# Optimization experiments

Measured on AMD Instinct MI355X. Metric: run time of the kernel, lower is better.

The kernel has to match this reference:

```python
import jax, jax.numpy as jnp
import numpy as np

N = 100_000   # nodes
E = 1_600_000 # edges
C = 64        # in = hidden = out channels
H = 8         # heads
D = C // H    # head_dim = 8
R = 4         # relations
L = 2         # layers


def setup_inputs() -> dict:
    key = jax.random.key(0)
    ks = jax.random.split(key, 10)
    sc = 1.0 / np.sqrt(C)  # xavier-ish scale
    return {
        "x": jax.random.normal(ks[0], (N, C), jnp.float32),
        "edge_index": jax.random.randint(ks[1], (2, E), 0, N),
        "edge_type": jax.random.randint(ks[2], (E,), 0, R),
        "W_Q": jax.random.normal(ks[3], (L, R, H, C, D), jnp.float32) * sc,
        "W_K": jax.random.normal(ks[4], (L, R, H, C, D), jnp.float32) * sc,
        "W_V": jax.random.normal(ks[5], (L, R, H, C, D), jnp.float32) * sc,
        "W_concat": jax.random.normal(ks[6], (L, R, H * D, C), jnp.float32) * sc,
        "sem_w": jax.random.normal(ks[7], (L, C), jnp.float32) * sc,
        "sem_b": jnp.zeros((L,), jnp.float32),
        "W_self": jax.random.normal(ks[8], (L, C, C), jnp.float32) * sc,
        "ln_g": jnp.ones((L, C), jnp.float32),
        "ln_b": jnp.zeros((L, C), jnp.float32),
    }


def _layer(x, src, dst, edge_type, WQ, WK, WV, Wcat, sw, sb, Ws, g, b):
    inv_sqrt_d = 1.0 / np.sqrt(D)
    rel_msgs = []
    for r in range(R):  # small fixed relation loop
        mask = (edge_type == r).astype(x.dtype)             # (E,)
        Q = jnp.einsum('nc,hcd->nhd', x, WQ[r])             # (N,H,D)
        K = jnp.einsum('nc,hcd->nhd', x, WK[r])
        V = jnp.einsum('nc,hcd->nhd', x, WV[r])
        # edge-wise QK energy, leaky_relu(0.01), scatter-add into dst node
        energy = jnp.einsum('ehd,ehd->eh', Q[dst], K[src]) * inv_sqrt_d
        energy = jax.nn.leaky_relu(energy)                  # (E,H)
        alpha_n = jax.ops.segment_sum(energy * mask[:, None], dst,
                                      num_segments=N)       # (N,H)
        alpha = jax.nn.softmax(alpha_n, axis=0)             # softmax over nodes
        w = alpha[dst] * mask[:, None]                      # (E,H)
        m = jax.ops.segment_sum(w[:, :, None] * V[src], dst,
                                num_segments=N)             # (N,H,D)
        rel_msgs.append(m.reshape(N, H * D) @ Wcat[r])      # (N,C)
    stacked = jnp.stack(rel_msgs)                           # (R,N,C)
    beta = jax.nn.softmax(stacked @ sw + sb, axis=0)        # (R,N) semantic attn
    agg = jnp.einsum('rn,rnc->nc', beta, stacked)           # (N,C)
    y = x + jax.nn.gelu(x @ Ws + agg, approximate=False)
    mu = y.mean(-1, keepdims=True)
    var = y.var(-1, keepdims=True)
    return (y - mu) / jnp.sqrt(var + 1e-5) * g + b


def reference(x, edge_index, edge_type, W_Q, W_K, W_V, W_concat,
              sem_w, sem_b, W_self, ln_g, ln_b):
    src, dst = edge_index[0], edge_index[1]  # PyG source_to_target: j=row0, i=row1
    for l in range(L):
        x = _layer(x, src, dst, edge_type, W_Q[l], W_K[l], W_V[l], W_concat[l],
                   sem_w[l], sem_b[l], W_self[l], ln_g[l], ln_b[l])
        # inter-layer dropout omitted (inference / eval mode)
    return x
```

## Files before the change

### kernel.cpp

```cpp
#include <hip/hip_runtime.h>
#include <hip/hip_bf16.h>

#define NN 100000
#define EE 1600000
#define RRR 4
#define HHH 8
#define NT 400000
#define GG 782
#define SHIFT 9
#define NBLK 512
#define CHUNK 3125
#define BMAX 2560

typedef unsigned int u32;
typedef unsigned short u16;
typedef __attribute__((ext_vector_type(8))) short bf16x8;
typedef __attribute__((ext_vector_type(4))) float f32x4;

static constexpr size_t OFF_KV   = 0;
static constexpr size_t OFF_Q    = 25600000;
static constexpr size_t OFF_S    = 76800000;
static constexpr size_t OFF_AL   = 128000000;
static constexpr size_t OFF_PW   = 140800000;
static constexpr size_t OFF_PART = 141100000;
static constexpr size_t OFF_FIN  = 141110000;
static constexpr size_t OFF_CW   = 141120000;
static constexpr size_t OFF_ROWP = 141365504;
static constexpr size_t OFF_EDG  = 142965512;
static constexpr size_t OFF_LG   = 149400000;
static constexpr size_t OFF_BSTORE = OFF_S;
static constexpr size_t OFF_HIST   = OFF_S + 8000000;
static constexpr size_t OFF_OFFA   = OFF_S + 16000000;
static constexpr size_t OFF_BASE   = OFF_S + 24000000;

__device__ inline u16 f2bf(float f){
  union { __hip_bfloat16 h; u16 u; } cv; cv.h = __float2bfloat16(f); return cv.u;
}
__device__ inline float bf2f(u16 u){ return __uint_as_float(((u32)u) << 16); }

__global__ __launch_bounds__(256) void k_histA(const int* __restrict__ dst, const int* __restrict__ typ,
                                               u32* __restrict__ Hist){
  __shared__ u32 h[GG];
  int b = blockIdx.x, t = threadIdx.x;
  for (int g = t; g < GG; g += 256) h[g] = 0u;
  __syncthreads();
  int e0 = b * CHUNK;
  for (int e = e0 + t; e < e0 + CHUNK; e += 256){
    int seg = typ[e] * NN + dst[e];
    atomicAdd(&h[seg >> SHIFT], 1u);
  }
  __syncthreads();
  for (int g = t; g < GG; g += 256) Hist[(size_t)b * GG + g] = h[g];
}

__global__ __launch_bounds__(1024) void k_base(const u32* __restrict__ Hist, u32* __restrict__ Base,
                                               u32* __restrict__ rowp){
  __shared__ u32 tot[GG];
  int t = threadIdx.x;
  if (t < GG){
    u32 s = 0;
    for (int b = 0; b < NBLK; b++) s += Hist[(size_t)b * GG + t];
    tot[t] = s;
  }
  __syncthreads();
  if (t == 0){
    u32 acc = 0;
    for (int g = 0; g < GG; g++){ u32 c = tot[g]; Base[g] = acc; acc += c; }
    Base[GG] = acc;
    rowp[NT] = EE;
  }
}

__global__ __launch_bounds__(512) void k_off(const u32* __restrict__ Hist, const u32* __restrict__ Base,
                                             u32* __restrict__ Off){
  __shared__ u32 v[NBLK];
  int g = blockIdx.x, t = threadIdx.x;
  v[t] = Hist[(size_t)t * GG + g];
  __syncthreads();
  if (t == 0){
    u32 acc = Base[g];
    for (int b = 0; b < NBLK; b++){ u32 c = v[b]; v[b] = acc; acc += c; }
  }
  __syncthreads();
  Off[(size_t)g * NBLK + t] = v[t];
}

__global__ __launch_bounds__(256) void k_fill(const int* __restrict__ src, const int* __restrict__ dst,
                                              const int* __restrict__ typ, const u32* __restrict__ Off,
                                              u32* __restrict__ bstore){
  __shared__ u32 cur[GG];
  int b = blockIdx.x, t = threadIdx.x;
  for (int g = t; g < GG; g += 256) cur[g] = Off[(size_t)g * NBLK + b];
  __syncthreads();
  int e0 = b * CHUNK;
  for (int e = e0 + t; e < e0 + CHUNK; e += 256){
    int seg = typ[e] * NN + dst[e];
    u32 pos = atomicAdd(&cur[seg >> SHIFT], 1u);
    bstore[pos] = ((u32)(seg & 511) << 17) | (u32)src[e];
  }
}

__global__ __launch_bounds__(256) void k_sortD(const u32* __restrict__ bstore, const u32* __restrict__ Base,
                                               u32* __restrict__ rowp, u32* __restrict__ edges){
  __shared__ u32 ent[BMAX];
  __shared__ u32 binc[512], bexc[512];
  int g = blockIdx.x, t = threadIdx.x;
  u32 base = Base[g];
  u32 cnt = Base[g + 1] - base;
  if (cnt > (u32)BMAX) cnt = (u32)BMAX;
  for (int i = t; i < 512; i += 256) binc[i] = 0u;
  __syncthreads();
  for (u32 i = t; i < cnt; i += 256){
    u32 v = bstore[base + i];
    ent[i] = v;
    atomicAdd(&binc[v >> 17], 1u);
  }
  __syncthreads();
  if (t == 0){
    u32 acc = 0;
    #pragma unroll 8
    for (int s = 0; s < 512; s++){ u32 c = binc[s]; bexc[s] = acc; binc[s] = acc; acc += c; }
  }
  __syncthreads();
  for (int s = t; s < 512; s += 256){
    int seg = g * 512 + s;
    if (seg < NT) rowp[seg] = base + bexc[s];
  }
  __syncthreads();
  for (u32 i = t; i < cnt; i += 256){
    u32 v = ent[i];
    u32 p = atomicAdd(&binc[v >> 17], 1u);
    edges[base + p] = v & 0x1FFFFu;
  }
}

__global__ __launch_bounds__(256) void k_repackbf(const float* __restrict__ WQ, const float* __restrict__ WK,
                                                  const float* __restrict__ WV, const float* __restrict__ Wcat,
                                                  const float* __restrict__ Wself, u16* __restrict__ pwB){
  int t = blockIdx.x * 256 + threadIdx.x;
  if (t >= 2 * 17 * 4096) return;
  int l = t / (17 * 4096), rem = t % (17 * 4096);
  int mat = rem >> 12, idx = rem & 4095;
  int out = idx >> 6, c = idx & 63;
  float v;
  if (mat < 12){
    int kind = mat >> 2, r = mat & 3;
    int h = out >> 3, d = out & 7;
    const float* Wsrc = (kind == 0) ? WQ : (kind == 1) ? WK : WV;
    v = Wsrc[((((l * RRR + r) * HHH + h) * 64) + c) * 8 + d];
  } else if (mat == 12){
    v = Wself[(l * 64 + c) * 64 + out];
  } else {
    int r = mat - 13;
    v = Wcat[(((l * RRR + r) * 64) + c) * 64 + out];
  }
  pwB[t] = f2bf(v);
}

__global__ __launch_bounds__(512) void k_cw(const float* __restrict__ Wcat, const float* __restrict__ semw,
                                            float* __restrict__ cw){
  int t = threadIdx.x;
  int l = t >> 8, r = (t >> 6) & 3, k = t & 63;
  const float* wp = Wcat + (((size_t)(l * RRR + r) * 64) + k) * 64;
  const float* sp = semw + l * 64;
  float s = 0.f;
  #pragma unroll 8
  for (int c = 0; c < 64; c++) s += wp[c] * sp[c];
  cw[t] = s;
}


__global__ __launch_bounds__(256) void k_qkv(const float* __restrict__ x,
                                             const u16* __restrict__ pwQ, const u16* __restrict__ pwK,
                                             const u16* __restrict__ pwV,
                                             u16* __restrict__ Qr, u32* __restrict__ kvp){
  __shared__ u16 xa[64][72];
  __shared__ u16 wt[3][64][72];
  int t = threadIdx.x;
  int n0 = blockIdx.x * 64;
  {
    int row = t >> 2, c0 = (t & 3) * 16;
    int n = n0 + row;
    float4 v0 = {}, v1 = {}, v2 = {}, v3 = {};
    if (n < NN){
      const float4* xp = (const float4*)(x + (size_t)n * 64 + c0);
      v0 = xp[0]; v1 = xp[1]; v2 = xp[2]; v3 = xp[3];
    }
    ushort4* dp = (ushort4*)&xa[row][c0];
    dp[0] = make_ushort4(f2bf(v0.x), f2bf(v0.y), f2bf(v0.z), f2bf(v0.w));
    dp[1] = make_ushort4(f2bf(v1.x), f2bf(v1.y), f2bf(v1.z), f2bf(v1.w));
    dp[2] = make_ushort4(f2bf(v2.x), f2bf(v2.y), f2bf(v2.z), f2bf(v2.w));
    dp[3] = make_ushort4(f2bf(v3.x), f2bf(v3.y), f2bf(v3.z), f2bf(v3.w));
  }
  {
    const u32* p0 = (const u32*)pwQ;
    const u32* p1 = (const u32*)pwK;
    const u32* p2 = (const u32*)pwV;
    for (int idx = t; idx < 3 * 2048; idx += 256){
      int m = idx >> 11, rem = idx & 2047;
      int out = rem >> 5, cc = rem & 31;
      u32 w = (m == 0) ? p0[rem] : (m == 1) ? p1[rem] : p2[rem];
      *(u32*)&wt[m][out][cc * 2] = w;
    }
  }
  __syncthreads();
  int w = t >> 6, lane = t & 63;
  int ra = w * 16 + (lane & 15);
  int kg = (lane >> 4) * 8;
  int cb = lane & 15;
  int rb = (lane >> 4) * 4;
  bf16x8 a0 = *(const bf16x8*)&xa[ra][kg];
  bf16x8 a1 = *(const bf16x8*)&xa[ra][32 + kg];
  f32x4 z = {0.f, 0.f, 0.f, 0.f};
  {
    f32x4 acc[4] = {z, z, z, z};
    #pragma unroll
    for (int t4 = 0; t4 < 4; t4++){
      bf16x8 b0 = *(const bf16x8*)&wt[0][t4 * 16 + cb][kg];
      bf16x8 b1 = *(const bf16x8*)&wt[0][t4 * 16 + cb][32 + kg];
      acc[t4] = __builtin_amdgcn_mfma_f32_16x16x32_bf16(a0, b0, acc[t4], 0, 0, 0);
      acc[t4] = __builtin_amdgcn_mfma_f32_16x16x32_bf16(a1, b1, acc[t4], 0, 0, 0);
    }
    #pragma unroll
    for (int t4 = 0; t4 < 4; t4++){
      #pragma unroll
      for (int i = 0; i < 4; i++){
        int n = n0 + w * 16 + rb + i;
        if (n < NN) Qr[(size_t)n * 64 + t4 * 16 + cb] = f2bf(acc[t4][i]);
      }
    }
  }
  {
    f32x4 ak[4] = {z, z, z, z};
    f32x4 av[4] = {z, z, z, z};
    #pragma unroll
    for (int t4 = 0; t4 < 4; t4++){
      bf16x8 bk0 = *(const bf16x8*)&wt[1][t4 * 16 + cb][kg];
      bf16x8 bk1 = *(const bf16x8*)&wt[1][t4 * 16 + cb][32 + kg];
      bf16x8 bv0 = *(const bf16x8*)&wt[2][t4 * 16 + cb][kg];
      bf16x8 bv1 = *(const bf16x8*)&wt[2][t4 * 16 + cb][32 + kg];
      ak[t4] = __builtin_amdgcn_mfma_f32_16x16x32_bf16(a0, bk0, ak[t4], 0, 0, 0);
      ak[t4] = __builtin_amdgcn_mfma_f32_16x16x32_bf16(a1, bk1, ak[t4], 0, 0, 0);
      av[t4] = __builtin_amdgcn_mfma_f32_16x16x32_bf16(a0, bv0, av[t4], 0, 0, 0);
      av[t4] = __builtin_amdgcn_mfma_f32_16x16x32_bf16(a1, bv1, av[t4], 0, 0, 0);
    }
    #pragma unroll
    for (int t4 = 0; t4 < 4; t4++){
      #pragma unroll
      for (int i = 0; i < 4; i++){
        int n = n0 + w * 16 + rb + i;
        if (n < NN) kvp[(size_t)n * 64 + t4 * 16 + cb] = (u32)f2bf(ak[t4][i]) | ((u32)f2bf(av[t4][i]) << 16);
      }
    }
  }
}

__global__ __launch_bounds__(256) void k_self(const float* __restrict__ x, const u16* __restrict__ pwS,
                                              u16* __restrict__ outb){
  __shared__ u16 xa[64][72];
  __shared__ u16 wt[64][72];
  int t = threadIdx.x;
  int n0 = blockIdx.x * 64;
  {
    int row = t >> 2, c0 = (t & 3) * 16;
    int n = n0 + row;
    float4 v0 = {}, v1 = {}, v2 = {}, v3 = {};
    if (n < NN){
      const float4* xp = (const float4*)(x + (size_t)n * 64 + c0);
      v0 = xp[0]; v1 = xp[1]; v2 = xp[2]; v3 = xp[3];
    }
    ushort4* dp = (ushort4*)&xa[row][c0];
    dp[0] = make_ushort4(f2bf(v0.x), f2bf(v0.y), f2bf(v0.z), f2bf(v0.w));
    dp[1] = make_ushort4(f2bf(v1.x), f2bf(v1.y), f2bf(v1.z), f2bf(v1.w));
    dp[2] = make_ushort4(f2bf(v2.x), f2bf(v2.y), f2bf(v2.z), f2bf(v2.w));
    dp[3] = make_ushort4(f2bf(v3.x), f2bf(v3.y), f2bf(v3.z), f2bf(v3.w));
  }
  {
    const u32* p0 = (const u32*)pwS;
    for (int idx = t; idx < 2048; idx += 256){
      int out = idx >> 5, cc = idx & 31;
      *(u32*)&wt[out][cc * 2] = p0[idx];
    }
  }
  __syncthreads();
  int w = t >> 6, lane = t & 63;
  int ra = w * 16 + (lane & 15);
  int kg = (lane >> 4) * 8;
  int cb = lane & 15;
  int rb = (lane >> 4) * 4;
  bf16x8 a0 = *(const bf16x8*)&xa[ra][kg];
  bf16x8 a1 = *(const bf16x8*)&xa[ra][32 + kg];
  f32x4 z = {0.f, 0.f, 0.f, 0.f};
  f32x4 acc[4] = {z, z, z, z};
  #pragma unroll
  for (int t4 = 0; t4 < 4; t4++){
    bf16x8 b0 = *(const bf16x8*)&wt[t4 * 16 + cb][kg];
    bf16x8 b1 = *(const bf16x8*)&wt[t4 * 16 + cb][32 + kg];
    acc[t4] = __builtin_amdgcn_mfma_f32_16x16x32_bf16(a0, b0, acc[t4], 0, 0, 0);
    acc[t4] = __builtin_amdgcn_mfma_f32_16x16x32_bf16(a1, b1, acc[t4], 0, 0, 0);
  }
  #pragma unroll
  for (int t4 = 0; t4 < 4; t4++){
    #pragma unroll
    for (int i = 0; i < 4; i++){
      int n = n0 + w * 16 + rb + i;
      if (n < NN) outb[(size_t)n * 64 + t4 * 16 + cb] = f2bf(acc[t4][i]);
    }
  }
}

__global__ __launch_bounds__(256) void k_gather(const u32* __restrict__ edges, const u32* __restrict__ rowpR,
                                                const u32* __restrict__ kvp, const u16* __restrict__ Qr,
                                                u16* __restrict__ Sr, float* __restrict__ alphaR){
  int wid = threadIdx.x >> 6, lane = threadIdx.x & 63;
  int half = lane >> 5;
  int i = lane & 31;
  int n = blockIdx.x * 4 + wid;
  u32 qp = *(const u32*)&Qr[(size_t)n * 64 + 2 * i];
  float q0 = bf2f((u16)(qp & 0xFFFFu));
  float q1 = bf2f((u16)(qp >> 16));
  u32 beg = rowpR[n], end = rowpR[n + 1];
  float sa0 = 0.f, sa1 = 0.f, aa = 0.f;
  const float isd = 0.35355339059327373f;
  for (u32 base = beg; base < end; base += 64){
    u32 cnt = (end - base < 64u) ? (end - base) : 64u;
    u32 eidx = (base + (u32)lane < end) ? edges[base + lane] : 0u;
    u32 j = 0;
    for (; j + 8 <= cnt; j += 8){
      int s0 = __shfl((int)eidx, (int)(j + half));
      int s1 = __shfl((int)eidx, (int)(j + 2 + half));
      int s2 = __shfl((int)eidx, (int)(j + 4 + half));
      int s3 = __shfl((int)eidx, (int)(j + 6 + half));
      uint2 w0 = *(const uint2*)&kvp[(size_t)s0 * 64 + 2 * i];
      uint2 w1 = *(const uint2*)&kvp[(size_t)s1 * 64 + 2 * i];
      uint2 w2 = *(const uint2*)&kvp[(size_t)s2 * 64 + 2 * i];
      uint2 w3 = *(const uint2*)&kvp[(size_t)s3 * 64 + 2 * i];
      float p0 = q0 * bf2f((u16)(w0.x & 0xFFFFu)) + q1 * bf2f((u16)(w0.y & 0xFFFFu));
      float p1 = q0 * bf2f((u16)(w1.x & 0xFFFFu)) + q1 * bf2f((u16)(w1.y & 0xFFFFu));
      float p2 = q0 * bf2f((u16)(w2.x & 0xFFFFu)) + q1 * bf2f((u16)(w2.y & 0xFFFFu));
      float p3 = q0 * bf2f((u16)(w3.x & 0xFFFFu)) + q1 * bf2f((u16)(w3.y & 0xFFFFu));
      p0 += __shfl_xor(p0, 1); p1 += __shfl_xor(p1, 1); p2 += __shfl_xor(p2, 1); p3 += __shfl_xor(p3, 1);
      p0 += __shfl_xor(p0, 2); p1 += __shfl_xor(p1, 2); p2 += __shfl_xor(p2, 2); p3 += __shfl_xor(p3, 2);
      float e0 = p0 * isd; e0 = (e0 > 0.f) ? e0 : 0.01f * e0;
      float e1 = p1 * isd; e1 = (e1 > 0.f) ? e1 : 0.01f * e1;
      float e2 = p2 * isd; e2 = (e2 > 0.f) ? e2 : 0.01f * e2;
      float e3 = p3 * isd; e3 = (e3 > 0.f) ? e3 : 0.01f * e3;
      aa += (e0 + e1) + (e2 + e3);
      sa0 += (bf2f((u16)(w0.x >> 16)) + bf2f((u16)(w1.x >> 16))) +
             (bf2f((u16)(w2.x >> 16)) + bf2f((u16)(w3.x >> 16)));
      sa1 += (bf2f((u16)(w0.y >> 16)) + bf2f((u16)(w1.y >> 16))) +
             (bf2f((u16)(w2.y >> 16)) + bf2f((u16)(w3.y >> 16)));
    }
    for (; j < cnt; j += 2){
      u32 jj = j + (u32)half;
      float mk = (jj < cnt) ? 1.f : 0.f;
      u32 js = (jj < cnt) ? jj : (cnt - 1);
      int s = __shfl((int)eidx, (int)js);
      uint2 w = *(const uint2*)&kvp[(size_t)s * 64 + 2 * i];
      float p = q0 * bf2f((u16)(w.x & 0xFFFFu)) + q1 * bf2f((u16)(w.y & 0xFFFFu));
      p += __shfl_xor(p, 1);
      p += __shfl_xor(p, 2);
      float e = p * isd; e = (e > 0.f) ? e : 0.01f * e;
      aa += e * mk;
      sa0 += bf2f((u16)(w.x >> 16)) * mk;
      sa1 += bf2f((u16)(w.y >> 16)) * mk;
    }
  }
  sa0 += __shfl_xor(sa0, 32);
  sa1 += __shfl_xor(sa1, 32);
  aa  += __shfl_xor(aa, 32);
  if (half == 0){
    ushort2 o; o.x = f2bf(sa0); o.y = f2bf(sa1);
    *(ushort2*)&Sr[(size_t)n * 64 + 2 * i] = o;
    if ((i & 3) == 0) alphaR[(size_t)n * 8 + (i >> 2)] = aa;
  }
}

__global__ __launch_bounds__(256) void k_stats1(const float* __restrict__ alpha, float2* __restrict__ part){
  int r = blockIdx.y;
  int chunk = blockIdx.x;
  const int per = (NN + 31) / 32;
  int nbeg = chunk * per;
  int nend = nbeg + per; if (nend > NN) nend = NN;
  int t = threadIdx.x;
  int h = t & 7;
  int g = t >> 3;
  float m = -1e30f, s = 0.f;
  for (int n = nbeg + g; n < nend; n += 32){
    float a = alpha[((size_t)r * NN + n) * 8 + h];
    if (a > m){ s *= expf(m - a); m = a; }
    s += expf(a - m);
  }
  __shared__ float sm[256], ss[256];
  sm[t] = m; ss[t] = s; __syncthreads();
  for (int off = 128; off >= 8; off >>= 1){
    if (t < off){
      float m2 = sm[t + off], s2 = ss[t + off];
      float M = fmaxf(sm[t], m2);
      ss[t] = ss[t] * expf(sm[t] - M) + s2 * expf(m2 - M);
      sm[t] = M;
    }
    __syncthreads();
  }
  if (t < 8) part[(r * 8 + t) * 32 + chunk] = make_float2(sm[t], ss[t]);
}

__global__ void k_stats2(const float2* __restrict__ part, float2* __restrict__ fin){
  int col = threadIdx.x;
  if (col < 32){
    float M = -1e30f, S = 0.f;
    for (int i = 0; i < 32; i++){
      float2 p = part[col * 32 + i];
      float Mn = fmaxf(M, p.x);
      S = S * expf(M - Mn) + p.y * expf(p.x - Mn);
      M = Mn;
    }
    fin[col] = make_float2(M, 1.f / S);
  }
}

__global__ __launch_bounds__(256) void k_msg(const u16* __restrict__ S, const float* __restrict__ alpha,
                                             const float2* __restrict__ fin, const u16* __restrict__ pwCat,
                                             const float* __restrict__ cwL, float* __restrict__ lgbuf,
                                             u16* __restrict__ stacked){
  __shared__ u16 xa[64][72];
  __shared__ u16 wt[64][72];
  int r = blockIdx.y;
  int t = threadIdx.x;
  int n0 = blockIdx.x * 64;
  {
    int row = t >> 2, c0 = (t & 3) * 16;
    int n = n0 + row;
    int na = (n < NN) ? n : (NN - 1);
    int h0 = c0 >> 3;
    float2 f0 = fin[r * 8 + h0];
    float2 f1 = fin[r * 8 + h0 + 1];
    float a0 = alpha[((size_t)r * NN + na) * 8 + h0];
    float a1 = alpha[((size_t)r * NN + na) * 8 + h0 + 1];
    float w0 = expf(a0 - f0.x) * f0.y;
    float w1 = expf(a1 - f1.x) * f1.y;
    const u32* sp = (const u32*)(S + ((size_t)r * NN + na) * 64 + c0);
    const float* cwr = cwL + r * 64;
    float lgp = 0.f;
    #pragma unroll
    for (int jj = 0; jj < 8; jj++){
      u32 bts = sp[jj];
      float wm = (jj < 4) ? w0 : w1;
      float mv0 = bf2f((u16)(bts & 0xFFFFu)) * wm;
      float mv1 = bf2f((u16)(bts >> 16)) * wm;
      lgp += mv0 * cwr[c0 + jj * 2] + mv1 * cwr[c0 + jj * 2 + 1];
      ushort2 o;
      o.x = f2bf(mv0);
      o.y = f2bf(mv1);
      *(ushort2*)&xa[row][c0 + jj * 2] = o;
    }
    lgp += __shfl_xor(lgp, 1);
    lgp += __shfl_xor(lgp, 2);
    if ((t & 3) == 0 && n < NN) lgbuf[(size_t)r * NN + n] = lgp;
  }
  {
    const u32* p0 = (const u32*)(pwCat + (size_t)r * 4096);
    for (int idx = t; idx < 2048; idx += 256){
      int out = idx >> 5, cc = idx & 31;
      *(u32*)&wt[out][cc * 2] = p0[idx];
    }
  }
  __syncthreads();
  int w = t >> 6, lane = t & 63;
  int ra = w * 16 + (lane & 15);
  int kg = (lane >> 4) * 8;
  int cb = lane & 15;
  int rb = (lane >> 4) * 4;
  bf16x8 a0 = *(const bf16x8*)&xa[ra][kg];
  bf16x8 a1 = *(const bf16x8*)&xa[ra][32 + kg];
  f32x4 z = {0.f, 0.f, 0.f, 0.f};
  f32x4 acc[4] = {z, z, z, z};
  #pragma unroll
  for (int t4 = 0; t4 < 4; t4++){
    bf16x8 b0 = *(const bf16x8*)&wt[t4 * 16 + cb][kg];
    bf16x8 b1 = *(const bf16x8*)&wt[t4 * 16 + cb][32 + kg];
    acc[t4] = __builtin_amdgcn_mfma_f32_16x16x32_bf16(a0, b0, acc[t4], 0, 0, 0);
    acc[t4] = __builtin_amdgcn_mfma_f32_16x16x32_bf16(a1, b1, acc[t4], 0, 0, 0);
  }
  #pragma unroll
  for (int t4 = 0; t4 < 4; t4++){
    #pragma unroll
    for (int i = 0; i < 4; i++){
      int n = n0 + w * 16 + rb + i;
      if (n < NN) stacked[((size_t)r * NN + n) * 64 + t4 * 16 + cb] = f2bf(acc[t4][i]);
    }
  }
}

__global__ __launch_bounds__(256) void k_final(const u16* __restrict__ stacked, const u16* __restrict__ selfb,
                                               const float* __restrict__ xin, const float* __restrict__ lgbuf,
                                               const float* __restrict__ lng, const float* __restrict__ lnb,
                                               float* __restrict__ xout){
  int t = threadIdx.x;
  int wid = t >> 6, lane = t & 63;
  int n = blockIdx.x * 4 + wid;
  float st[4];
  #pragma unroll
  for (int r = 0; r < 4; r++) st[r] = bf2f(stacked[((size_t)r * NN + n) * 64 + lane]);
  float lg0 = lgbuf[n];
  float lg1 = lgbuf[(size_t)NN + n];
  float lg2 = lgbuf[(size_t)2 * NN + n];
  float lg3 = lgbuf[(size_t)3 * NN + n];
  float mx = fmaxf(fmaxf(lg0, lg1), fmaxf(lg2, lg3));
  float e0 = expf(lg0 - mx), e1 = expf(lg1 - mx), e2 = expf(lg2 - mx), e3 = expf(lg3 - mx);
  float inv = 1.f / (e0 + e1 + e2 + e3);
  float agg = (e0 * st[0] + e1 * st[1] + e2 * st[2] + e3 * st[3]) * inv;
  float pre = bf2f(selfb[(size_t)n * 64 + lane]) + agg;
  float ge = 0.5f * pre * (1.f + erff(pre * 0.70710678118654752f));
  float y = xin[(size_t)n * 64 + lane] + ge;
  float mu = y;
  #pragma unroll
  for (int o = 1; o < 64; o <<= 1) mu += __shfl_xor(mu, o);
  mu *= (1.f / 64.f);
  float d = y - mu;
  float vv = d * d;
  #pragma unroll
  for (int o = 1; o < 64; o <<= 1) vv += __shfl_xor(vv, o);
  vv *= (1.f / 64.f);
  xout[(size_t)n * 64 + lane] = d * rsqrtf(vv + 1e-5f) * lng[lane] + lnb[lane];
}

extern "C" void kernel_launch(void* const* d_in, const int* in_sizes, int n_in,
                              void* d_out, int out_size, void* d_ws, size_t ws_size,
                              hipStream_t stream){
  const float* x0    = (const float*)d_in[0];
  const int*   eidx  = (const int*)d_in[1];
  const int*   etyp  = (const int*)d_in[2];
  const float* WQ    = (const float*)d_in[3];
  const float* WK    = (const float*)d_in[4];
  const float* WV    = (const float*)d_in[5];
  const float* Wcat  = (const float*)d_in[6];
  const float* semw  = (const float*)d_in[7];
  const float* semb  = (const float*)d_in[8];
  const float* Wself = (const float*)d_in[9];
  const float* lng   = (const float*)d_in[10];
  const float* lnb   = (const float*)d_in[11];
  float* out = (float*)d_out;
  char* ws = (char*)d_ws;

  const int* srcArr = eidx;
  const int* dstArr = eidx + EE;

  u32*  kvp      = (u32*)(ws + OFF_KV);
  u16*  selfb    = (u16*)(ws + OFF_KV);
  u16*  Qb       = (u16*)(ws + OFF_Q);
  u16*  stackedB = (u16*)(ws + OFF_Q);
  u16*  Sb       = (u16*)(ws + OFF_S);
  float* alphaB  = (float*)(ws + OFF_AL);
  u16*  pwB      = (u16*)(ws + OFF_PW);
  float2* part   = (float2*)(ws + OFF_PART);
  float2* fin    = (float2*)(ws + OFF_FIN);
  float* cw      = (float*)(ws + OFF_CW);
  float* lgbuf   = (float*)(ws + OFF_LG);
  u32* rowp   = (u32*)(ws + OFF_ROWP);
  u32* edges  = (u32*)(ws + OFF_EDG);
  u32* bstore = (u32*)(ws + OFF_BSTORE);
  u32* Hist   = (u32*)(ws + OFF_HIST);
  u32* Off    = (u32*)(ws + OFF_OFFA);
  u32* Base   = (u32*)(ws + OFF_BASE);

  k_histA<<<NBLK, 256, 0, stream>>>(dstArr, etyp, Hist);
  k_base<<<1, 1024, 0, stream>>>(Hist, Base, rowp);
  k_off<<<GG, 512, 0, stream>>>(Hist, Base, Off);
  k_fill<<<NBLK, 256, 0, stream>>>(srcArr, dstArr, etyp, Off, bstore);
  k_sortD<<<GG, 256, 0, stream>>>(bstore, Base, rowp, edges);
  k_repackbf<<<(2 * 17 * 4096 + 255) / 256, 256, 0, stream>>>(WQ, WK, WV, Wcat, Wself, pwB);
  k_cw<<<1, 512, 0, stream>>>(Wcat, semw, cw);

  for (int l = 0; l < 2; l++){
    const float* xcur = (l == 0) ? x0 : out;
    const u16* pwL = pwB + (size_t)l * 17 * 4096;
    for (int r = 0; r < 4; r++){
      k_qkv<<<1563, 256, 0, stream>>>(xcur, pwL + (size_t)r * 4096, pwL + (size_t)(4 + r) * 4096,
                                      pwL + (size_t)(8 + r) * 4096, Qb + (size_t)r * NN * 64, kvp);
      k_gather<<<NN / 4, 256, 0, stream>>>(edges, rowp + (size_t)r * NN, kvp,
                                           Qb + (size_t)r * NN * 64,
                                           Sb + (size_t)r * NN * 64,
                                           alphaB + (size_t)r * NN * 8);
    }
    k_self<<<1563, 256, 0, stream>>>(xcur, pwL + (size_t)12 * 4096, selfb);
    k_stats1<<<dim3(32, 4), 256, 0, stream>>>(alphaB, part);
    k_stats2<<<1, 64, 0, stream>>>(part, fin);
    k_msg<<<dim3(1563, 4), 256, 0, stream>>>(Sb, alphaB, fin, pwL + (size_t)13 * 4096,
                                             cw + l * 256, lgbuf, stackedB);
    k_final<<<NN / 4, 256, 0, stream>>>(stackedB, selfb, xcur, lgbuf,
                                        lng + l * 64, lnb + l * 64, out);
  }
  (void)in_sizes; (void)n_in; (void)out_size; (void)ws_size;
  (void)semb;
}
```

Baseline: 726.7 us.

## Fuse per-relation QKV and self projections into one kernel, batch gathers

Merges the four per-relation QKV launches and the self-projection launch into a single kernel. It reads x once per tile and takes weight fragments straight from global memory instead of staging them in LDS. K/V buffers are now kept for all four relations at once, so a single gather kernel loops over relations inside each wave. This removes eight launches and several redundant reads of x per layer, but roughly quadruples the K/V workspace. The larger per-relation working set may hurt cache locality in the gather.

```diff
diff --git a/kernel.cpp b/kernel.cpp
--- a/kernel.cpp
+++ b/kernel.cpp
@@ -18,16 +18,17 @@
 typedef __attribute__((ext_vector_type(4))) float f32x4;
 
 static constexpr size_t OFF_KV   = 0;
-static constexpr size_t OFF_Q    = 25600000;
-static constexpr size_t OFF_S    = 76800000;
-static constexpr size_t OFF_AL   = 128000000;
-static constexpr size_t OFF_PW   = 140800000;
-static constexpr size_t OFF_PART = 141100000;
-static constexpr size_t OFF_FIN  = 141110000;
-static constexpr size_t OFF_CW   = 141120000;
-static constexpr size_t OFF_ROWP = 141365504;
-static constexpr size_t OFF_EDG  = 142965512;
-static constexpr size_t OFF_LG   = 149400000;
+static constexpr size_t OFF_Q    = 102400000;
+static constexpr size_t OFF_S    = 153600000;
+static constexpr size_t OFF_SELF = 204800000;
+static constexpr size_t OFF_AL   = 217600000;
+static constexpr size_t OFF_PW   = 230400000;
+static constexpr size_t OFF_PART = 230700000;
+static constexpr size_t OFF_FIN  = 230710000;
+static constexpr size_t OFF_CW   = 230720000;
+static constexpr size_t OFF_LG   = 230730000;
+static constexpr size_t OFF_ROWP = 232400000;
+static constexpr size_t OFF_EDG  = 234100000;
 static constexpr size_t OFF_BSTORE = OFF_S;
 static constexpr size_t OFF_HIST   = OFF_S + 8000000;
 static constexpr size_t OFF_OFFA   = OFF_S + 16000000;
@@ -170,12 +171,10 @@
 }
 
 
-__global__ __launch_bounds__(256) void k_qkv(const float* __restrict__ x,
-                                             const u16* __restrict__ pwQ, const u16* __restrict__ pwK,
-                                             const u16* __restrict__ pwV,
-                                             u16* __restrict__ Qr, u32* __restrict__ kvp){
+__global__ __launch_bounds__(256) void k_qkvself(const float* __restrict__ x, const u16* __restrict__ pwL,
+                                                 u16* __restrict__ QAll, u16* __restrict__ selfb,
+                                                 u32* __restrict__ kvpAll){
   __shared__ u16 xa[64][72];
-  __shared__ u16 wt[3][64][72];
   int t = threadIdx.x;
   int n0 = blockIdx.x * 64;
   {
@@ -192,17 +191,6 @@
     dp[2] = make_ushort4(f2bf(v2.x), f2bf(v2.y), f2bf(v2.z), f2bf(v2.w));
     dp[3] = make_ushort4(f2bf(v3.x), f2bf(v3.y), f2bf(v3.z), f2bf(v3.w));
   }
-  {
-    const u32* p0 = (const u32*)pwQ;
-    const u32* p1 = (const u32*)pwK;
-    const u32* p2 = (const u32*)pwV;
-    for (int idx = t; idx < 3 * 2048; idx += 256){
-      int m = idx >> 11, rem = idx & 2047;
-      int out = rem >> 5, cc = rem & 31;
-      u32 w = (m == 0) ? p0[rem] : (m == 1) ? p1[rem] : p2[rem];
-      *(u32*)&wt[m][out][cc * 2] = w;
-    }
-  }
   __syncthreads();
   int w = t >> 6, lane = t & 63;
   int ra = w * 16 + (lane & 15);
@@ -212,167 +200,123 @@
   bf16x8 a0 = *(const bf16x8*)&xa[ra][kg];
   bf16x8 a1 = *(const bf16x8*)&xa[ra][32 + kg];
   f32x4 z = {0.f, 0.f, 0.f, 0.f};
-  {
+  #pragma unroll
+  for (int m = 0; m < 5; m++){
+    const u16* wp = pwL + (size_t)((m < 4) ? m : 12) * 4096;
     f32x4 acc[4] = {z, z, z, z};
     #pragma unroll
     for (int t4 = 0; t4 < 4; t4++){
-      bf16x8 b0 = *(const bf16x8*)&wt[0][t4 * 16 + cb][kg];
-      bf16x8 b1 = *(const bf16x8*)&wt[0][t4 * 16 + cb][32 + kg];
+      bf16x8 b0 = *(const bf16x8*)(wp + (t4 * 16 + cb) * 64 + kg);
+      bf16x8 b1 = *(const bf16x8*)(wp + (t4 * 16 + cb) * 64 + 32 + kg);
       acc[t4] = __builtin_amdgcn_mfma_f32_16x16x32_bf16(a0, b0, acc[t4], 0, 0, 0);
       acc[t4] = __builtin_amdgcn_mfma_f32_16x16x32_bf16(a1, b1, acc[t4], 0, 0, 0);
     }
+    u16* op = (m < 4) ? (QAll + (size_t)m * NN * 64) : selfb;
     #pragma unroll
     for (int t4 = 0; t4 < 4; t4++){
       #pragma unroll
-      for (int i = 0; i < 4; i++){
-        int n = n0 + w * 16 + rb + i;
-        if (n < NN) Qr[(size_t)n * 64 + t4 * 16 + cb] = f2bf(acc[t4][i]);
+      for (int i2 = 0; i2 < 4; i2++){
+        int n = n0 + w * 16 + rb + i2;
+        if (n < NN) op[(size_t)n * 64 + t4 * 16 + cb] = f2bf(acc[t4][i2]);
       }
     }
   }
-  {
+  #pragma unroll
+  for (int r = 0; r < 4; r++){
+    const u16* wk = pwL + (size_t)(4 + r) * 4096;
+    const u16* wv = pwL + (size_t)(8 + r) * 4096;
     f32x4 ak[4] = {z, z, z, z};
     f32x4 av[4] = {z, z, z, z};
     #pragma unroll
     for (int t4 = 0; t4 < 4; t4++){
-      bf16x8 bk0 = *(const bf16x8*)&wt[1][t4 * 16 + cb][kg];
-      bf16x8 bk1 = *(const bf16x8*)&wt[1][t4 * 16 + cb][32 + kg];
-      bf16x8 bv0 = *(const bf16x8*)&wt[2][t4 * 16 + cb][kg];
-      bf16x8 bv1 = *(const bf16x8*)&wt[2][t4 * 16 + cb][32 + kg];
+      bf16x8 bk0 = *(const bf16x8*)(wk + (t4 * 16 + cb) * 64 + kg);
+      bf16x8 bk1 = *(const bf16x8*)(wk + (t4 * 16 + cb) * 64 + 32 + kg);
+      bf16x8 bv0 = *(const bf16x8*)(wv + (t4 * 16 + cb) * 64 + kg);
+      bf16x8 bv1 = *(const bf16x8*)(wv + (t4 * 16 + cb) * 64 + 32 + kg);
       ak[t4] = __builtin_amdgcn_mfma_f32_16x16x32_bf16(a0, bk0, ak[t4], 0, 0, 0);
       ak[t4] = __builtin_amdgcn_mfma_f32_16x16x32_bf16(a1, bk1, ak[t4], 0, 0, 0);
       av[t4] = __builtin_amdgcn_mfma_f32_16x16x32_bf16(a0, bv0, av[t4], 0, 0, 0);
       av[t4] = __builtin_amdgcn_mfma_f32_16x16x32_bf16(a1, bv1, av[t4], 0, 0, 0);
     }
+    u32* kp = kvpAll + (size_t)r * NN * 64;
     #pragma unroll
     for (int t4 = 0; t4 < 4; t4++){
       #pragma unroll
-      for (int i = 0; i < 4; i++){
-        int n = n0 + w * 16 + rb + i;
-        if (n < NN) kvp[(size_t)n * 64 + t4 * 16 + cb] = (u32)f2bf(ak[t4][i]) | ((u32)f2bf(av[t4][i]) << 16);
+      for (int i2 = 0; i2 < 4; i2++){
+        int n = n0 + w * 16 + rb + i2;
+        if (n < NN) kp[(size_t)n * 64 + t4 * 16 + cb] = (u32)f2bf(ak[t4][i2]) | ((u32)f2bf(av[t4][i2]) << 16);
       }
     }
   }
 }
 
-__global__ __launch_bounds__(256) void k_self(const float* __restrict__ x, const u16* __restrict__ pwS,
-                                              u16* __restrict__ outb){
-  __shared__ u16 xa[64][72];
-  __shared__ u16 wt[64][72];
-  int t = threadIdx.x;
-  int n0 = blockIdx.x * 64;
-  {
-    int row = t >> 2, c0 = (t & 3) * 16;
-    int n = n0 + row;
-    float4 v0 = {}, v1 = {}, v2 = {}, v3 = {};
-    if (n < NN){
-      const float4* xp = (const float4*)(x + (size_t)n * 64 + c0);
-      v0 = xp[0]; v1 = xp[1]; v2 = xp[2]; v3 = xp[3];
-    }
-    ushort4* dp = (ushort4*)&xa[row][c0];
-    dp[0] = make_ushort4(f2bf(v0.x), f2bf(v0.y), f2bf(v0.z), f2bf(v0.w));
-    dp[1] = make_ushort4(f2bf(v1.x), f2bf(v1.y), f2bf(v1.z), f2bf(v1.w));
-    dp[2] = make_ushort4(f2bf(v2.x), f2bf(v2.y), f2bf(v2.z), f2bf(v2.w));
-    dp[3] = make_ushort4(f2bf(v3.x), f2bf(v3.y), f2bf(v3.z), f2bf(v3.w));
-  }
-  {
-    const u32* p0 = (const u32*)pwS;
-    for (int idx = t; idx < 2048; idx += 256){
-      int out = idx >> 5, cc = idx & 31;
-      *(u32*)&wt[out][cc * 2] = p0[idx];
-    }
-  }
-  __syncthreads();
-  int w = t >> 6, lane = t & 63;
-  int ra = w * 16 + (lane & 15);
-  int kg = (lane >> 4) * 8;
-  int cb = lane & 15;
-  int rb = (lane >> 4) * 4;
-  bf16x8 a0 = *(const bf16x8*)&xa[ra][kg];
-  bf16x8 a1 = *(const bf16x8*)&xa[ra][32 + kg];
-  f32x4 z = {0.f, 0.f, 0.f, 0.f};
-  f32x4 acc[4] = {z, z, z, z};
-  #pragma unroll
-  for (int t4 = 0; t4 < 4; t4++){
-    bf16x8 b0 = *(const bf16x8*)&wt[t4 * 16 + cb][kg];
-    bf16x8 b1 = *(const bf16x8*)&wt[t4 * 16 + cb][32 + kg];
-    acc[t4] = __builtin_amdgcn_mfma_f32_16x16x32_bf16(a0, b0, acc[t4], 0, 0, 0);
-    acc[t4] = __builtin_amdgcn_mfma_f32_16x16x32_bf16(a1, b1, acc[t4], 0, 0, 0);
-  }
-  #pragma unroll
-  for (int t4 = 0; t4 < 4; t4++){
-    #pragma unroll
-    for (int i = 0; i < 4; i++){
-      int n = n0 + w * 16 + rb + i;
-      if (n < NN) outb[(size_t)n * 64 + t4 * 16 + cb] = f2bf(acc[t4][i]);
-    }
-  }
-}
-
-__global__ __launch_bounds__(256) void k_gather(const u32* __restrict__ edges, const u32* __restrict__ rowpR,
-                                                const u32* __restrict__ kvp, const u16* __restrict__ Qr,
-                                                u16* __restrict__ Sr, float* __restrict__ alphaR){
+__global__ __launch_bounds__(256) void k_gather4(const u32* __restrict__ edges, const u32* __restrict__ rowp,
+                                                 const u32* __restrict__ kvpAll, const u16* __restrict__ QAll,
+                                                 u16* __restrict__ Sb, float* __restrict__ alphaB){
   int wid = threadIdx.x >> 6, lane = threadIdx.x & 63;
   int half = lane >> 5;
   int i = lane & 31;
   int n = blockIdx.x * 4 + wid;
-  u32 qp = *(const u32*)&Qr[(size_t)n * 64 + 2 * i];
-  float q0 = bf2f((u16)(qp & 0xFFFFu));
-  float q1 = bf2f((u16)(qp >> 16));
-  u32 beg = rowpR[n], end = rowpR[n + 1];
-  float sa0 = 0.f, sa1 = 0.f, aa = 0.f;
   const float isd = 0.35355339059327373f;
-  for (u32 base = beg; base < end; base += 64){
-    u32 cnt = (end - base < 64u) ? (end - base) : 64u;
-    u32 eidx = (base + (u32)lane < end) ? edges[base + lane] : 0u;
-    u32 j = 0;
-    for (; j + 8 <= cnt; j += 8){
-      int s0 = __shfl((int)eidx, (int)(j + half));
-      int s1 = __shfl((int)eidx, (int)(j + 2 + half));
-      int s2 = __shfl((int)eidx, (int)(j + 4 + half));
-      int s3 = __shfl((int)eidx, (int)(j + 6 + half));
-      uint2 w0 = *(const uint2*)&kvp[(size_t)s0 * 64 + 2 * i];
-      uint2 w1 = *(const uint2*)&kvp[(size_t)s1 * 64 + 2 * i];
-      uint2 w2 = *(const uint2*)&kvp[(size_t)s2 * 64 + 2 * i];
-      uint2 w3 = *(const uint2*)&kvp[(size_t)s3 * 64 + 2 * i];
-      float p0 = q0 * bf2f((u16)(w0.x & 0xFFFFu)) + q1 * bf2f((u16)(w0.y & 0xFFFFu));
-      float p1 = q0 * bf2f((u16)(w1.x & 0xFFFFu)) + q1 * bf2f((u16)(w1.y & 0xFFFFu));
-      float p2 = q0 * bf2f((u16)(w2.x & 0xFFFFu)) + q1 * bf2f((u16)(w2.y & 0xFFFFu));
-      float p3 = q0 * bf2f((u16)(w3.x & 0xFFFFu)) + q1 * bf2f((u16)(w3.y & 0xFFFFu));
-      p0 += __shfl_xor(p0, 1); p1 += __shfl_xor(p1, 1); p2 += __shfl_xor(p2, 1); p3 += __shfl_xor(p3, 1);
-      p0 += __shfl_xor(p0, 2); p1 += __shfl_xor(p1, 2); p2 += __shfl_xor(p2, 2); p3 += __shfl_xor(p3, 2);
-      float e0 = p0 * isd; e0 = (e0 > 0.f) ? e0 : 0.01f * e0;
-      float e1 = p1 * isd; e1 = (e1 > 0.f) ? e1 : 0.01f * e1;
-      float e2 = p2 * isd; e2 = (e2 > 0.f) ? e2 : 0.01f * e2;
-      float e3 = p3 * isd; e3 = (e3 > 0.f) ? e3 : 0.01f * e3;
-      aa += (e0 + e1) + (e2 + e3);
-      sa0 += (bf2f((u16)(w0.x >> 16)) + bf2f((u16)(w1.x >> 16))) +
-             (bf2f((u16)(w2.x >> 16)) + bf2f((u16)(w3.x >> 16)));
-      sa1 += (bf2f((u16)(w0.y >> 16)) + bf2f((u16)(w1.y >> 16))) +
-             (bf2f((u16)(w2.y >> 16)) + bf2f((u16)(w3.y >> 16)));
-    }
-    for (; j < cnt; j += 2){
-      u32 jj = j + (u32)half;
-      float mk = (jj < cnt) ? 1.f : 0.f;
-      u32 js = (jj < cnt) ? jj : (cnt - 1);
-      int s = __shfl((int)eidx, (int)js);
-      uint2 w = *(const uint2*)&kvp[(size_t)s * 64 + 2 * i];
-      float p = q0 * bf2f((u16)(w.x & 0xFFFFu)) + q1 * bf2f((u16)(w.y & 0xFFFFu));
-      p += __shfl_xor(p, 1);
-      p += __shfl_xor(p, 2);
-      float e = p * isd; e = (e > 0.f) ? e : 0.01f * e;
-      aa += e * mk;
-      sa0 += bf2f((u16)(w.x >> 16)) * mk;
-      sa1 += bf2f((u16)(w.y >> 16)) * mk;
-    }
-  }
-  sa0 += __shfl_xor(sa0, 32);
-  sa1 += __shfl_xor(sa1, 32);
-  aa  += __shfl_xor(aa, 32);
-  if (half == 0){
-    ushort2 o; o.x = f2bf(sa0); o.y = f2bf(sa1);
-    *(ushort2*)&Sr[(size_t)n * 64 + 2 * i] = o;
-    if ((i & 3) == 0) alphaR[(size_t)n * 8 + (i >> 2)] = aa;
+  for (int r = 0; r < 4; r++){
+    const u32* kvp = kvpAll + (size_t)r * NN * 64;
+    u32 qp = *(const u32*)&QAll[((size_t)r * NN + n) * 64 + 2 * i];
+    float q0 = bf2f((u16)(qp & 0xFFFFu));
+    float q1 = bf2f((u16)(qp >> 16));
+    u32 beg = rowp[(size_t)r * NN + n], end = rowp[(size_t)r * NN + n + 1];
+    float sa0 = 0.f, sa1 = 0.f, aa = 0.f;
+    for (u32 base = beg; base < end; base += 64){
+      u32 cnt = (end - base < 64u) ? (end - base) : 64u;
+      u32 eidx = (base + (u32)lane < end) ? edges[base + lane] : 0u;
+      u32 j = 0;
+      for (; j + 8 <= cnt; j += 8){
+        int s0 = __shfl((int)eidx, (int)(j + half));
+        int s1 = __shfl((int)eidx, (int)(j + 2 + half));
+        int s2 = __shfl((int)eidx, (int)(j + 4 + half));
+        int s3 = __shfl((int)eidx, (int)(j + 6 + half));
+        uint2 w0 = *(const uint2*)&kvp[(size_t)s0 * 64 + 2 * i];
+        uint2 w1 = *(const uint2*)&kvp[(size_t)s1 * 64 + 2 * i];
+        uint2 w2 = *(const uint2*)&kvp[(size_t)s2 * 64 + 2 * i];
+        uint2 w3 = *(const uint2*)&kvp[(size_t)s3 * 64 + 2 * i];
+        float p0 = q0 * bf2f((u16)(w0.x & 0xFFFFu)) + q1 * bf2f((u16)(w0.y & 0xFFFFu));
+        float p1 = q0 * bf2f((u16)(w1.x & 0xFFFFu)) + q1 * bf2f((u16)(w1.y & 0xFFFFu));
+        float p2 = q0 * bf2f((u16)(w2.x & 0xFFFFu)) + q1 * bf2f((u16)(w2.y & 0xFFFFu));
+        float p3 = q0 * bf2f((u16)(w3.x & 0xFFFFu)) + q1 * bf2f((u16)(w3.y & 0xFFFFu));
+        p0 += __shfl_xor(p0, 1); p1 += __shfl_xor(p1, 1); p2 += __shfl_xor(p2, 1); p3 += __shfl_xor(p3, 1);
+        p0 += __shfl_xor(p0, 2); p1 += __shfl_xor(p1, 2); p2 += __shfl_xor(p2, 2); p3 += __shfl_xor(p3, 2);
+        float e0 = p0 * isd; e0 = (e0 > 0.f) ? e0 : 0.01f * e0;
+        float e1 = p1 * isd; e1 = (e1 > 0.f) ? e1 : 0.01f * e1;
+        float e2 = p2 * isd; e2 = (e2 > 0.f) ? e2 : 0.01f * e2;
+        float e3 = p3 * isd; e3 = (e3 > 0.f) ? e3 : 0.01f * e3;
+        aa += (e0 + e1) + (e2 + e3);
+        sa0 += (bf2f((u16)(w0.x >> 16)) + bf2f((u16)(w1.x >> 16))) +
+               (bf2f((u16)(w2.x >> 16)) + bf2f((u16)(w3.x >> 16)));
+        sa1 += (bf2f((u16)(w0.y >> 16)) + bf2f((u16)(w1.y >> 16))) +
+               (bf2f((u16)(w2.y >> 16)) + bf2f((u16)(w3.y >> 16)));
+      }
+      for (; j < cnt; j += 2){
+        u32 jj = j + (u32)half;
+        float mk = (jj < cnt) ? 1.f : 0.f;
+        u32 js = (jj < cnt) ? jj : (cnt - 1);
+        int s = __shfl((int)eidx, (int)js);
+        uint2 w = *(const uint2*)&kvp[(size_t)s * 64 + 2 * i];
+        float p = q0 * bf2f((u16)(w.x & 0xFFFFu)) + q1 * bf2f((u16)(w.y & 0xFFFFu));
+        p += __shfl_xor(p, 1);
+        p += __shfl_xor(p, 2);
+        float e = p * isd; e = (e > 0.f) ? e : 0.01f * e;
+        aa += e * mk;
+        sa0 += bf2f((u16)(w.x >> 16)) * mk;
+        sa1 += bf2f((u16)(w.y >> 16)) * mk;
+      }
+    }
+    sa0 += __shfl_xor(sa0, 32);
+    sa1 += __shfl_xor(sa1, 32);
+    aa  += __shfl_xor(aa, 32);
+    if (half == 0){
+      ushort2 o; o.x = f2bf(sa0); o.y = f2bf(sa1);
+      *(ushort2*)&Sb[((size_t)r * NN + n) * 64 + 2 * i] = o;
+      if ((i & 3) == 0) alphaB[((size_t)r * NN + n) * 8 + (i >> 2)] = aa;
+    }
   }
 }
 
@@ -546,11 +490,11 @@
   const int* srcArr = eidx;
   const int* dstArr = eidx + EE;
 
-  u32*  kvp      = (u32*)(ws + OFF_KV);
-  u16*  selfb    = (u16*)(ws + OFF_KV);
+  u32*  kvpAll   = (u32*)(ws + OFF_KV);
   u16*  Qb       = (u16*)(ws + OFF_Q);
   u16*  stackedB = (u16*)(ws + OFF_Q);
   u16*  Sb       = (u16*)(ws + OFF_S);
+  u16*  selfb    = (u16*)(ws + OFF_SELF);
   float* alphaB  = (float*)(ws + OFF_AL);
   u16*  pwB      = (u16*)(ws + OFF_PW);
   float2* part   = (float2*)(ws + OFF_PART);
@@ -575,15 +519,8 @@
   for (int l = 0; l < 2; l++){
     const float* xcur = (l == 0) ? x0 : out;
     const u16* pwL = pwB + (size_t)l * 17 * 4096;
-    for (int r = 0; r < 4; r++){
-      k_qkv<<<1563, 256, 0, stream>>>(xcur, pwL + (size_t)r * 4096, pwL + (size_t)(4 + r) * 4096,
-                                      pwL + (size_t)(8 + r) * 4096, Qb + (size_t)r * NN * 64, kvp);
-      k_gather<<<NN / 4, 256, 0, stream>>>(edges, rowp + (size_t)r * NN, kvp,
-                                           Qb + (size_t)r * NN * 64,
-                                           Sb + (size_t)r * NN * 64,
-                                           alphaB + (size_t)r * NN * 8);
-    }
-    k_self<<<1563, 256, 0, stream>>>(xcur, pwL + (size_t)12 * 4096, selfb);
+    k_qkvself<<<1563, 256, 0, stream>>>(xcur, pwL, Qb, selfb, kvpAll);
+    k_gather4<<<NN / 4, 256, 0, stream>>>(edges, rowp, kvpAll, Qb, Sb, alphaB);
     k_stats1<<<dim3(32, 4), 256, 0, stream>>>(alphaB, part);
     k_stats2<<<1, 64, 0, stream>>>(part, fin);
     k_msg<<<dim3(1563, 4), 256, 0, stream>>>(Sb, alphaB, fin, pwL + (size_t)13 * 4096,
```

Result: slower. 742.8 us (+2.2%).
